# Kernel tuning notes

Hardware: AMD Instinct MI355X
Metric: run time of the kernel (lower is better)

The kernel has to match this reference:

```python
import jax, jax.numpy as jnp
import numpy as np

N_NODES = 100000
N_EDGES = 600000
C_IN, C_HID, C_OUT = 256, 128, 128
LN_EPS = 1e-5
NEG_SLOPE = 0.01  # nn.LeakyReLU default


def setup_inputs() -> dict:
    key = jax.random.key(0)
    ks = jax.random.split(key, 9)
    x = jax.random.normal(ks[0], (N_NODES, C_IN), dtype=jnp.float32)
    x_struct = jax.random.normal(ks[1], (1,), dtype=jnp.float32)  # unused by forward
    x_e = jax.random.normal(ks[2], (1,), dtype=jnp.float32)       # unused by forward
    edge_index = jax.random.randint(ks[3], (2, N_EDGES), 0, N_NODES, dtype=jnp.int64)
    W1 = jax.random.normal(ks[4], (C_IN, C_HID), dtype=jnp.float32) / np.sqrt(C_IN)
    b1 = jnp.zeros((C_HID,), dtype=jnp.float32)
    gamma = jnp.ones((C_HID,), dtype=jnp.float32)
    beta = jnp.zeros((C_HID,), dtype=jnp.float32)
    W2 = jax.random.normal(ks[5], (C_HID, C_OUT), dtype=jnp.float32) / np.sqrt(C_HID)
    b2 = jnp.zeros((C_OUT,), dtype=jnp.float32)
    return {"x": x, "x_struct": x_struct, "x_e": x_e, "edge_index": edge_index,
            "W1": W1, "b1": b1, "gamma": gamma, "beta": beta, "W2": W2, "b2": b2}


def reference(x, x_struct, x_e, edge_index, W1, b1, gamma, beta, W2, b2):
    # dropout is identity in eval mode
    h = jax.nn.leaky_relu(x @ W1 + b1, negative_slope=NEG_SLOPE)  # [N, H]
    # LayerNorm over last dim
    mu = jnp.mean(h, axis=-1, keepdims=True)
    var = jnp.mean(jnp.square(h - mu), axis=-1, keepdims=True)
    h = (h - mu) * jax.lax.rsqrt(var + LN_EPS) * gamma + beta
    # gather source-node features, scatter-min into destination nodes
    src, dst = edge_index[0], edge_index[1]
    msgs = h[src]                                                 # [E, H]
    agg = jax.ops.segment_min(msgs, dst, num_segments=N_NODES)   # empty -> +inf
    counts = jax.ops.segment_sum(jnp.ones((msgs.shape[0],), dtype=jnp.float32),
                                 dst, num_segments=N_NODES)
    agg = jnp.where(counts[:, None] > 0, agg, 0.0)               # PyG fills empty with 0
    return agg @ W2 + b2                                          # [N, C_OUT]
```

## Files before the change

kernel.cpp:

```cpp
#include <hip/hip_runtime.h>
#include <hip/hip_bf16.h>
#include <cstdint>

#define N_NODES 100000
#define N_EDGES 600000
#define C_IN    256
#define C_HID   128
#define C_OUT   128
#define LN_EPS  1e-5f
#define NEG_SLOPE 0.01f

#define NSCAN_BLOCKS 391

typedef float f32x4 __attribute__((ext_vector_type(4)));
typedef __attribute__((ext_vector_type(8))) short frag_ab;

__device__ __forceinline__ void split2(float f, ushort& h, ushort& l) {
    unsigned u = __float_as_uint(f);
    h = (ushort)(u >> 16);
    float d = f - __uint_as_float(u & 0xFFFF0000u);
    l = (ushort)(__float_as_uint(d) >> 16);
}

__device__ __forceinline__ void split8(const float4& p, const float4& q,
                                       frag_ab& hi, frag_ab& lo) {
    ushort h, l;
    split2(p.x, h, l); hi[0] = (short)h; lo[0] = (short)l;
    split2(p.y, h, l); hi[1] = (short)h; lo[1] = (short)l;
    split2(p.z, h, l); hi[2] = (short)h; lo[2] = (short)l;
    split2(p.w, h, l); hi[3] = (short)h; lo[3] = (short)l;
    split2(q.x, h, l); hi[4] = (short)h; lo[4] = (short)l;
    split2(q.y, h, l); hi[5] = (short)h; lo[5] = (short)l;
    split2(q.z, h, l); hi[6] = (short)h; lo[6] = (short)l;
    split2(q.w, h, l); hi[7] = (short)h; lo[7] = (short)l;
}

__device__ __forceinline__ void stage_w_chunk(const float* __restrict__ Wk,
                                              ushort* __restrict__ sW, int tid) {
    #pragma unroll
    for (int it = 0; it < 16; ++it) {
        int id = it * 256 + tid;
        int n  = id & 127;
        int kg = id >> 7;
        float w0 = Wk[(kg * 4 + 0) * 128 + n];
        float w1 = Wk[(kg * 4 + 1) * 128 + n];
        float w2 = Wk[(kg * 4 + 2) * 128 + n];
        float w3 = Wk[(kg * 4 + 3) * 128 + n];
        ushort h0, h1, h2, h3, l0, l1, l2, l3;
        split2(w0, h0, l0); split2(w1, h1, l1);
        split2(w2, h2, l2); split2(w3, h3, l3);
        int bbyte = n * 256 + ((kg * 8) ^ ((n & 7) << 4));
        *(ushort4*)((char*)sW + bbyte)         = make_ushort4(h0, h1, h2, h3);
        *(ushort4*)((char*)sW + 65536 + bbyte) = make_ushort4(l0, l1, l2, l3);
    }
}

__global__ __launch_bounds__(256) void zero_kernel(int* __restrict__ p, int n) {
    int i = blockIdx.x * 256 + threadIdx.x;
    if (i < n) p[i] = 0;
}

__global__ __launch_bounds__(256) void hist_kernel(const int* __restrict__ ei,
                                                   int* __restrict__ deg) {
    int t = blockIdx.x * 256 + threadIdx.x;
    if (t < N_EDGES) atomicAdd(&deg[ei[N_EDGES + t]], 1);
}

__global__ __launch_bounds__(256) void block_sum_kernel(const int* __restrict__ deg,
                                                        int* __restrict__ bsum) {
    __shared__ int s[256];
    int i = blockIdx.x * 256 + threadIdx.x;
    s[threadIdx.x] = (i < N_NODES) ? deg[i] : 0;
    __syncthreads();
    #pragma unroll
    for (int o = 128; o > 0; o >>= 1) {
        if (threadIdx.x < o) s[threadIdx.x] += s[threadIdx.x + o];
        __syncthreads();
    }
    if (threadIdx.x == 0) bsum[blockIdx.x] = s[0];
}

__global__ __launch_bounds__(512) void scan_bsum_kernel(const int* __restrict__ bsum,
                                                        int* __restrict__ bpre,
                                                        int* __restrict__ offsets) {
    __shared__ int bufA[512], bufB[512];
    int t = threadIdx.x;
    int v = (t < NSCAN_BLOCKS) ? bsum[t] : 0;
    bufA[t] = v;
    __syncthreads();
    int* src = bufA; int* dst = bufB;
    #pragma unroll
    for (int o = 1; o < 512; o <<= 1) {
        dst[t] = src[t] + ((t >= o) ? src[t - o] : 0);
        __syncthreads();
        int* tmp = src; src = dst; dst = tmp;
    }
    if (t < NSCAN_BLOCKS) bpre[t] = src[t] - v;
    if (t == 0) offsets[N_NODES] = N_EDGES;
}

__global__ __launch_bounds__(256) void scan_block_kernel(const int* __restrict__ deg,
                                                         const int* __restrict__ bpre,
                                                         int* __restrict__ offsets) {
    __shared__ int bufA[256], bufB[256];
    int t = threadIdx.x;
    int i = blockIdx.x * 256 + t;
    int v = (i < N_NODES) ? deg[i] : 0;
    bufA[t] = v;
    __syncthreads();
    int* src = bufA; int* dst = bufB;
    #pragma unroll
    for (int o = 1; o < 256; o <<= 1) {
        dst[t] = src[t] + ((t >= o) ? src[t - o] : 0);
        __syncthreads();
        int* tmp = src; src = dst; dst = tmp;
    }
    if (i < N_NODES) offsets[i] = bpre[blockIdx.x] + src[t] - v;
}

__global__ __launch_bounds__(256) void csr_scatter_kernel(const int* __restrict__ ei,
                                                          const int* __restrict__ offsets,
                                                          int* __restrict__ cursor,
                                                          int* __restrict__ csr) {
    int t = blockIdx.x * 256 + threadIdx.x;
    if (t < N_EDGES) {
        int src = ei[t];
        int dst = ei[N_EDGES + t];
        int pos = atomicAdd(&cursor[dst], 1);
        csr[offsets[dst] + pos] = src;
    }
}

__global__ __launch_bounds__(256, 2) void gemm1_ln_mfma_kernel(
    const float* __restrict__ x, const float* __restrict__ W1,
    const float* __restrict__ b1, const float* __restrict__ gamma,
    const float* __restrict__ beta, float* __restrict__ h)
{
    __shared__ ushort sW[2 * 128 * 128];

    const int tid  = threadIdx.x;
    const int lane = tid & 63;
    const int wv   = tid >> 6;
    const int r16  = lane & 15;
    const int g    = lane >> 4;
    const int row0 = blockIdx.x * 128;

    f32x4 acc[2][8];
    #pragma unroll
    for (int mf = 0; mf < 2; ++mf)
        #pragma unroll
        for (int nf = 0; nf < 8; ++nf)
            acc[mf][nf] = (f32x4){0.f, 0.f, 0.f, 0.f};

    float b1v[8], gv[8], bv[8];
    #pragma unroll
    for (int nf = 0; nf < 8; ++nf) {
        int cidx = nf * 16 + r16;
        b1v[nf] = b1[cidx]; gv[nf] = gamma[cidx]; bv[nf] = beta[cidx];
    }

    const char* bbase = (const char*)sW + r16 * 256;
    const int swz = (lane & 7) << 4;

    for (int kc = 0; kc < 2; ++kc) {
        float4 araw[2][4][2];
        #pragma unroll
        for (int mf = 0; mf < 2; ++mf) {
            int r_a = row0 + wv * 32 + mf * 16 + r16;
            r_a = (r_a < N_NODES) ? r_a : (N_NODES - 1);
            const float* xp = x + (size_t)r_a * C_IN + kc * 128 + g * 8;
            #pragma unroll
            for (int ks = 0; ks < 4; ++ks) {
                araw[mf][ks][0] = *(const float4*)(xp + ks * 32);
                araw[mf][ks][1] = *(const float4*)(xp + ks * 32 + 4);
            }
        }

        stage_w_chunk(W1 + (size_t)kc * 128 * 128, sW, tid);
        __syncthreads();

        #pragma unroll
        for (int ks = 0; ks < 4; ++ks) {
            frag_ab aHi[2], aLo[2];
            split8(araw[0][ks][0], araw[0][ks][1], aHi[0], aLo[0]);
            split8(araw[1][ks][0], araw[1][ks][1], aHi[1], aLo[1]);
            const int kpart = (ks * 64 + g * 16) ^ swz;
            #pragma unroll
            for (int nf = 0; nf < 8; ++nf) {
                frag_ab bHi = *(const frag_ab*)(bbase + nf * 4096 + kpart);
                frag_ab bLo = *(const frag_ab*)(bbase + nf * 4096 + kpart + 65536);
                acc[0][nf] = __builtin_amdgcn_mfma_f32_16x16x32_bf16(aHi[0], bHi, acc[0][nf], 0, 0, 0);
                acc[0][nf] = __builtin_amdgcn_mfma_f32_16x16x32_bf16(aLo[0], bHi, acc[0][nf], 0, 0, 0);
                acc[0][nf] = __builtin_amdgcn_mfma_f32_16x16x32_bf16(aHi[0], bLo, acc[0][nf], 0, 0, 0);
                acc[1][nf] = __builtin_amdgcn_mfma_f32_16x16x32_bf16(aHi[1], bHi, acc[1][nf], 0, 0, 0);
                acc[1][nf] = __builtin_amdgcn_mfma_f32_16x16x32_bf16(aLo[1], bHi, acc[1][nf], 0, 0, 0);
                acc[1][nf] = __builtin_amdgcn_mfma_f32_16x16x32_bf16(aHi[1], bLo, acc[1][nf], 0, 0, 0);
            }
        }
        __syncthreads();
    }

    #pragma unroll
    for (int mf = 0; mf < 2; ++mf)
        #pragma unroll
        for (int nf = 0; nf < 8; ++nf)
            #pragma unroll
            for (int rg = 0; rg < 4; ++rg) {
                float v = acc[mf][nf][rg] + b1v[nf];
                acc[mf][nf][rg] = (v > 0.f) ? v : NEG_SLOPE * v;
            }

    #pragma unroll
    for (int mf = 0; mf < 2; ++mf) {
        #pragma unroll
        for (int rg = 0; rg < 4; ++rg) {
            float s = 0.f, ss = 0.f;
            #pragma unroll
            for (int nf = 0; nf < 8; ++nf) {
                float v = acc[mf][nf][rg];
                s += v; ss += v * v;
            }
            #pragma unroll
            for (int m = 1; m < 16; m <<= 1) {
                s  += __shfl_xor(s,  m, 64);
                ss += __shfl_xor(ss, m, 64);
            }
            float mu   = s * (1.f / C_HID);
            float var  = ss * (1.f / C_HID) - mu * mu;
            float rstd = rsqrtf(var + LN_EPS);
            int row = row0 + wv * 32 + mf * 16 + (g << 2) + rg;
            if (row < N_NODES) {
                #pragma unroll
                for (int nf = 0; nf < 8; ++nf) {
                    float o = (acc[mf][nf][rg] - mu) * rstd * gv[nf] + bv[nf];
                    h[(size_t)row * C_HID + nf * 16 + r16] = o;
                }
            }
        }
    }
}

__global__ __launch_bounds__(256) void gather_min_kernel(
    const float* __restrict__ h, const int* __restrict__ offsets,
    const int* __restrict__ csr, float* __restrict__ agg)
{
    const int lane = threadIdx.x & 63;
    const int row  = blockIdx.x * 4 + (threadIdx.x >> 6);
    if (row >= N_NODES) return;

    const int beg = offsets[row];
    const int end = offsets[row + 1];

    float m0 = INFINITY, m1 = INFINITY;

    for (int j0 = beg; j0 < end; j0 += 64) {
        const int cnt = min(64, end - j0);
        int idx = (lane < cnt) ? csr[j0 + lane] : 0;
        for (int k = 0; k < cnt; k += 4) {
            int s0 = __shfl(idx, k + 0);
            int s1 = __shfl(idx, k + 1);
            int s2 = __shfl(idx, k + 2);
            int s3 = __shfl(idx, k + 3);
            float2 v0 = ((const float2*)(h + (size_t)s0 * C_HID))[lane];
            float2 v1 = make_float2(INFINITY, INFINITY);
            float2 v2 = make_float2(INFINITY, INFINITY);
            float2 v3 = make_float2(INFINITY, INFINITY);
            if (k + 1 < cnt) v1 = ((const float2*)(h + (size_t)s1 * C_HID))[lane];
            if (k + 2 < cnt) v2 = ((const float2*)(h + (size_t)s2 * C_HID))[lane];
            if (k + 3 < cnt) v3 = ((const float2*)(h + (size_t)s3 * C_HID))[lane];
            m0 = fminf(fminf(m0, v0.x), fminf(fminf(v1.x, v2.x), v3.x));
            m1 = fminf(fminf(m1, v0.y), fminf(fminf(v1.y, v2.y), v3.y));
        }
    }

    if (m0 == INFINITY) m0 = 0.f;
    if (m1 == INFINITY) m1 = 0.f;
    ((float2*)(agg + (size_t)row * C_HID))[lane] = make_float2(m0, m1);
}

__global__ __launch_bounds__(256, 2) void gemm2_mfma_kernel(
    const float* __restrict__ agg, const float* __restrict__ W2,
    const float* __restrict__ b2, float* __restrict__ out)
{
    __shared__ ushort sW[2 * 128 * 128];

    const int tid  = threadIdx.x;
    const int lane = tid & 63;
    const int wv   = tid >> 6;
    const int r16  = lane & 15;
    const int g    = lane >> 4;
    const int row0 = blockIdx.x * 128;

    f32x4 acc[2][8];
    #pragma unroll
    for (int mf = 0; mf < 2; ++mf)
        #pragma unroll
        for (int nf = 0; nf < 8; ++nf)
            acc[mf][nf] = (f32x4){0.f, 0.f, 0.f, 0.f};

    float b2v[8];
    #pragma unroll
    for (int nf = 0; nf < 8; ++nf) b2v[nf] = b2[nf * 16 + r16];

    float4 araw[2][4][2];
    #pragma unroll
    for (int mf = 0; mf < 2; ++mf) {
        int r_a = row0 + wv * 32 + mf * 16 + r16;
        r_a = (r_a < N_NODES) ? r_a : (N_NODES - 1);
        const float* ap = agg + (size_t)r_a * C_HID + g * 8;
        #pragma unroll
        for (int ks = 0; ks < 4; ++ks) {
            araw[mf][ks][0] = *(const float4*)(ap + ks * 32);
            araw[mf][ks][1] = *(const float4*)(ap + ks * 32 + 4);
        }
    }

    stage_w_chunk(W2, sW, tid);
    __syncthreads();

    const char* bbase = (const char*)sW + r16 * 256;
    const int swz = (lane & 7) << 4;

    #pragma unroll
    for (int ks = 0; ks < 4; ++ks) {
        frag_ab aHi[2], aLo[2];
        split8(araw[0][ks][0], araw[0][ks][1], aHi[0], aLo[0]);
        split8(araw[1][ks][0], araw[1][ks][1], aHi[1], aLo[1]);
        const int kpart = (ks * 64 + g * 16) ^ swz;
        #pragma unroll
        for (int nf = 0; nf < 8; ++nf) {
            frag_ab bHi = *(const frag_ab*)(bbase + nf * 4096 + kpart);
            frag_ab bLo = *(const frag_ab*)(bbase + nf * 4096 + kpart + 65536);
            acc[0][nf] = __builtin_amdgcn_mfma_f32_16x16x32_bf16(aHi[0], bHi, acc[0][nf], 0, 0, 0);
            acc[0][nf] = __builtin_amdgcn_mfma_f32_16x16x32_bf16(aLo[0], bHi, acc[0][nf], 0, 0, 0);
            acc[0][nf] = __builtin_amdgcn_mfma_f32_16x16x32_bf16(aHi[0], bLo, acc[0][nf], 0, 0, 0);
            acc[1][nf] = __builtin_amdgcn_mfma_f32_16x16x32_bf16(aHi[1], bHi, acc[1][nf], 0, 0, 0);
            acc[1][nf] = __builtin_amdgcn_mfma_f32_16x16x32_bf16(aLo[1], bHi, acc[1][nf], 0, 0, 0);
            acc[1][nf] = __builtin_amdgcn_mfma_f32_16x16x32_bf16(aHi[1], bLo, acc[1][nf], 0, 0, 0);
        }
    }

    #pragma unroll
    for (int mf = 0; mf < 2; ++mf) {
        #pragma unroll
        for (int rg = 0; rg < 4; ++rg) {
            int row = row0 + wv * 32 + mf * 16 + (g << 2) + rg;
            if (row < N_NODES) {
                #pragma unroll
                for (int nf = 0; nf < 8; ++nf)
                    out[(size_t)row * C_OUT + nf * 16 + r16] = acc[mf][nf][rg] + b2v[nf];
            }
        }
    }
}

extern "C" void kernel_launch(void* const* d_in, const int* in_sizes, int n_in,
                              void* d_out, int out_size, void* d_ws, size_t ws_size,
                              hipStream_t stream)
{
    const float* x     = (const float*)d_in[0];
    const int*   ei    = (const int*)d_in[3];
    const float* W1    = (const float*)d_in[4];
    const float* b1    = (const float*)d_in[5];
    const float* gamma = (const float*)d_in[6];
    const float* beta  = (const float*)d_in[7];
    const float* W2    = (const float*)d_in[8];
    const float* b2    = (const float*)d_in[9];
    float*       out   = (float*)d_out;

    char* p = (char*)d_ws;
    float* h       = (float*)p;            p += (size_t)N_NODES * C_HID * 4;
    float* agg     = (float*)p;            p += (size_t)N_NODES * C_HID * 4;
    int*   deg     = (int*)p;              p += 400000;
    int*   cursor  = (int*)p;              p += 400000;
    int*   offsets = (int*)p;              p += 400016;
    int*   bsum    = (int*)p;              p += 1600;
    int*   bpre    = (int*)p;              p += 1600;
    int*   csr     = (int*)p;

    const int grid_e    = (N_EDGES + 255) / 256;
    const int grid_gemm = (N_NODES + 127) / 128;

    zero_kernel<<<(2 * N_NODES + 255) / 256, 256, 0, stream>>>(deg, 2 * N_NODES);
    hist_kernel<<<grid_e, 256, 0, stream>>>(ei, deg);
    block_sum_kernel<<<NSCAN_BLOCKS, 256, 0, stream>>>(deg, bsum);
    scan_bsum_kernel<<<1, 512, 0, stream>>>(bsum, bpre, offsets);
    scan_block_kernel<<<NSCAN_BLOCKS, 256, 0, stream>>>(deg, bpre, offsets);
    csr_scatter_kernel<<<grid_e, 256, 0, stream>>>(ei, offsets, cursor, csr);
    gemm1_ln_mfma_kernel<<<grid_gemm, 256, 0, stream>>>(x, W1, b1, gamma, beta, h);
    gather_min_kernel<<<(N_NODES + 3) / 4, 256, 0, stream>>>(h, offsets, csr, agg);
    gemm2_mfma_kernel<<<grid_gemm, 256, 0, stream>>>(agg, W2, b2, out);
}
```

Measured before the change: 354.4 us.

## Presplit weights into MFMA fragment layout once and load B from global

Adds a small kernel that splits W1 and W2 into bf16 hi/lo pairs once per call, already laid out in MFMA fragment order in workspace. The two GEMM kernels then read B fragments straight from global/L2 instead of every block re-splitting the weights into LDS. This removes the per-block staging work, the LDS buffer and the barriers, and the launch bound is raised to allow 3 blocks per CU. The trade is that B fragments are now fetched from cache memory on every MFMA step rather than from LDS, which could add latency and L2 traffic.

```diff
diff --git a/kernel.cpp b/kernel.cpp
--- a/kernel.cpp
+++ b/kernel.cpp
@@ -35,24 +35,33 @@
     split2(q.w, h, l); hi[7] = (short)h; lo[7] = (short)l;
 }
 
-__device__ __forceinline__ void stage_w_chunk(const float* __restrict__ Wk,
-                                              ushort* __restrict__ sW, int tid) {
-    #pragma unroll
-    for (int it = 0; it < 16; ++it) {
-        int id = it * 256 + tid;
-        int n  = id & 127;
-        int kg = id >> 7;
-        float w0 = Wk[(kg * 4 + 0) * 128 + n];
-        float w1 = Wk[(kg * 4 + 1) * 128 + n];
-        float w2 = Wk[(kg * 4 + 2) * 128 + n];
-        float w3 = Wk[(kg * 4 + 3) * 128 + n];
-        ushort h0, h1, h2, h3, l0, l1, l2, l3;
-        split2(w0, h0, l0); split2(w1, h1, l1);
-        split2(w2, h2, l2); split2(w3, h3, l3);
-        int bbyte = n * 256 + ((kg * 8) ^ ((n & 7) << 4));
-        *(ushort4*)((char*)sW + bbyte)         = make_ushort4(h0, h1, h2, h3);
-        *(ushort4*)((char*)sW + 65536 + bbyte) = make_ushort4(l0, l1, l2, l3);
-    }
+__global__ __launch_bounds__(256) void presplit_w_kernel(
+    const float* __restrict__ W1, const float* __restrict__ W2,
+    ushort* __restrict__ w1s, ushort* __restrict__ w2s)
+{
+    int tg = blockIdx.x * 256 + threadIdx.x;
+    const float* W; ushort* out; int t;
+    if (tg < 4096)      { W = W1; out = w1s; t = tg; }
+    else if (tg < 6144) { W = W2; out = w2s; t = tg - 4096; }
+    else return;
+
+    int lane = t & 63;
+    int ks   = (t >> 6) & 3;
+    int nf   = (t >> 8) & 7;
+    int kc   = t >> 11;
+    int k0   = kc * 128 + ks * 32 + (lane >> 4) * 8;
+    int n    = nf * 16 + (lane & 15);
+
+    frag_ab hi, lo;
+    #pragma unroll
+    for (int j = 0; j < 8; ++j) {
+        ushort h, l;
+        split2(W[(size_t)(k0 + j) * 128 + n], h, l);
+        hi[j] = (short)h; lo[j] = (short)l;
+    }
+    size_t fbase = (size_t)((kc * 32 + nf * 4 + ks) * 2) * 64 + lane;
+    ((frag_ab*)out)[fbase]      = hi;
+    ((frag_ab*)out)[fbase + 64] = lo;
 }
 
 __global__ __launch_bounds__(256) void zero_kernel(int* __restrict__ p, int n) {
@@ -131,13 +140,11 @@
     }
 }
 
-__global__ __launch_bounds__(256, 2) void gemm1_ln_mfma_kernel(
-    const float* __restrict__ x, const float* __restrict__ W1,
+__global__ __launch_bounds__(256, 3) void gemm1_ln_mfma_kernel(
+    const float* __restrict__ x, const ushort* __restrict__ w1s,
     const float* __restrict__ b1, const float* __restrict__ gamma,
     const float* __restrict__ beta, float* __restrict__ h)
 {
-    __shared__ ushort sW[2 * 128 * 128];
-
     const int tid  = threadIdx.x;
     const int lane = tid & 63;
     const int wv   = tid >> 6;
@@ -145,6 +152,8 @@
     const int g    = lane >> 4;
     const int row0 = blockIdx.x * 128;
 
+    const frag_ab* B1 = (const frag_ab*)w1s;
+
     f32x4 acc[2][8];
     #pragma unroll
     for (int mf = 0; mf < 2; ++mf)
@@ -159,9 +168,7 @@
         b1v[nf] = b1[cidx]; gv[nf] = gamma[cidx]; bv[nf] = beta[cidx];
     }
 
-    const char* bbase = (const char*)sW + r16 * 256;
-    const int swz = (lane & 7) << 4;
-
+    #pragma unroll
     for (int kc = 0; kc < 2; ++kc) {
         float4 araw[2][4][2];
         #pragma unroll
@@ -176,19 +183,16 @@
             }
         }
 
-        stage_w_chunk(W1 + (size_t)kc * 128 * 128, sW, tid);
-        __syncthreads();
-
         #pragma unroll
         for (int ks = 0; ks < 4; ++ks) {
             frag_ab aHi[2], aLo[2];
             split8(araw[0][ks][0], araw[0][ks][1], aHi[0], aLo[0]);
             split8(araw[1][ks][0], araw[1][ks][1], aHi[1], aLo[1]);
-            const int kpart = (ks * 64 + g * 16) ^ swz;
+            const int fb = (kc * 32 + ks) * 128 + lane;
             #pragma unroll
             for (int nf = 0; nf < 8; ++nf) {
-                frag_ab bHi = *(const frag_ab*)(bbase + nf * 4096 + kpart);
-                frag_ab bLo = *(const frag_ab*)(bbase + nf * 4096 + kpart + 65536);
+                frag_ab bHi = B1[fb + nf * 512];
+                frag_ab bLo = B1[fb + nf * 512 + 64];
                 acc[0][nf] = __builtin_amdgcn_mfma_f32_16x16x32_bf16(aHi[0], bHi, acc[0][nf], 0, 0, 0);
                 acc[0][nf] = __builtin_amdgcn_mfma_f32_16x16x32_bf16(aLo[0], bHi, acc[0][nf], 0, 0, 0);
                 acc[0][nf] = __builtin_amdgcn_mfma_f32_16x16x32_bf16(aHi[0], bLo, acc[0][nf], 0, 0, 0);
@@ -197,7 +201,6 @@
                 acc[1][nf] = __builtin_amdgcn_mfma_f32_16x16x32_bf16(aHi[1], bLo, acc[1][nf], 0, 0, 0);
             }
         }
-        __syncthreads();
     }
 
     #pragma unroll
@@ -278,12 +281,10 @@
     ((float2*)(agg + (size_t)row * C_HID))[lane] = make_float2(m0, m1);
 }
 
-__global__ __launch_bounds__(256, 2) void gemm2_mfma_kernel(
-    const float* __restrict__ agg, const float* __restrict__ W2,
+__global__ __launch_bounds__(256, 3) void gemm2_mfma_kernel(
+    const float* __restrict__ agg, const ushort* __restrict__ w2s,
     const float* __restrict__ b2, float* __restrict__ out)
 {
-    __shared__ ushort sW[2 * 128 * 128];
-
     const int tid  = threadIdx.x;
     const int lane = tid & 63;
     const int wv   = tid >> 6;
@@ -291,6 +292,8 @@
     const int g    = lane >> 4;
     const int row0 = blockIdx.x * 128;
 
+    const frag_ab* B2 = (const frag_ab*)w2s;
+
     f32x4 acc[2][8];
     #pragma unroll
     for (int mf = 0; mf < 2; ++mf)
@@ -315,22 +318,16 @@
         }
     }
 
-    stage_w_chunk(W2, sW, tid);
-    __syncthreads();
-
-    const char* bbase = (const char*)sW + r16 * 256;
-    const int swz = (lane & 7) << 4;
-
     #pragma unroll
     for (int ks = 0; ks < 4; ++ks) {
         frag_ab aHi[2], aLo[2];
         split8(araw[0][ks][0], araw[0][ks][1], aHi[0], aLo[0]);
         split8(araw[1][ks][0], araw[1][ks][1], aHi[1], aLo[1]);
-        const int kpart = (ks * 64 + g * 16) ^ swz;
+        const int fb = ks * 128 + lane;
         #pragma unroll
         for (int nf = 0; nf < 8; ++nf) {
-            frag_ab bHi = *(const frag_ab*)(bbase + nf * 4096 + kpart);
-            frag_ab bLo = *(const frag_ab*)(bbase + nf * 4096 + kpart + 65536);
+            frag_ab bHi = B2[fb + nf * 512];
+            frag_ab bLo = B2[fb + nf * 512 + 64];
             acc[0][nf] = __builtin_amdgcn_mfma_f32_16x16x32_bf16(aHi[0], bHi, acc[0][nf], 0, 0, 0);
             acc[0][nf] = __builtin_amdgcn_mfma_f32_16x16x32_bf16(aLo[0], bHi, acc[0][nf], 0, 0, 0);
             acc[0][nf] = __builtin_amdgcn_mfma_f32_16x16x32_bf16(aHi[0], bLo, acc[0][nf], 0, 0, 0);
@@ -369,25 +366,28 @@
     float*       out   = (float*)d_out;
 
     char* p = (char*)d_ws;
-    float* h       = (float*)p;            p += (size_t)N_NODES * C_HID * 4;
-    float* agg     = (float*)p;            p += (size_t)N_NODES * C_HID * 4;
-    int*   deg     = (int*)p;              p += 400000;
-    int*   cursor  = (int*)p;              p += 400000;
-    int*   offsets = (int*)p;              p += 400016;
-    int*   bsum    = (int*)p;              p += 1600;
-    int*   bpre    = (int*)p;              p += 1600;
-    int*   csr     = (int*)p;
+    float*  h       = (float*)p;           p += (size_t)N_NODES * C_HID * 4;
+    float*  agg     = (float*)p;           p += (size_t)N_NODES * C_HID * 4;
+    int*    deg     = (int*)p;             p += 400000;
+    int*    cursor  = (int*)p;             p += 400000;
+    int*    offsets = (int*)p;             p += 400016;
+    int*    bsum    = (int*)p;             p += 1600;
+    int*    bpre    = (int*)p;             p += 1600;
+    int*    csr     = (int*)p;             p += (size_t)N_EDGES * 4;
+    ushort* w1s     = (ushort*)p;          p += 131072;
+    ushort* w2s     = (ushort*)p;
 
     const int grid_e    = (N_EDGES + 255) / 256;
     const int grid_gemm = (N_NODES + 127) / 128;
 
+    presplit_w_kernel<<<24, 256, 0, stream>>>(W1, W2, w1s, w2s);
     zero_kernel<<<(2 * N_NODES + 255) / 256, 256, 0, stream>>>(deg, 2 * N_NODES);
     hist_kernel<<<grid_e, 256, 0, stream>>>(ei, deg);
     block_sum_kernel<<<NSCAN_BLOCKS, 256, 0, stream>>>(deg, bsum);
     scan_bsum_kernel<<<1, 512, 0, stream>>>(bsum, bpre, offsets);
     scan_block_kernel<<<NSCAN_BLOCKS, 256, 0, stream>>>(deg, bpre, offsets);
     csr_scatter_kernel<<<grid_e, 256, 0, stream>>>(ei, offsets, cursor, csr);
-    gemm1_ln_mfma_kernel<<<grid_gemm, 256, 0, stream>>>(x, W1, b1, gamma, beta, h);
+    gemm1_ln_mfma_kernel<<<grid_gemm, 256, 0, stream>>>(x, w1s, b1, gamma, beta, h);
     gather_min_kernel<<<(N_NODES + 3) / 4, 256, 0, stream>>>(h, offsets, csr, agg);
-    gemm2_mfma_kernel<<<grid_gemm, 256, 0, stream>>>(agg, W2, b2, out);
-}
+    gemm2_mfma_kernel<<<grid_gemm, 256, 0, stream>>>(agg, w2s, b2, out);
+}
```

Result: slower. 386.6 us (+9.1%).
